# Kernel optimization log

Hardware: AMD Instinct MI355X
Metric: run time of the kernel (lower is better)

The kernel has to match this reference:

```python
import jax, jax.numpy as jnp
import numpy as np

N_NODES = 50000
N_EDGES = 1600000
IN_DIM = 256
HID = 128
BATCH = 16384
EDGE_FEAT = 6
BN_EPS = 1e-5


def _glorot(key, shape):
    fan_in, fan_out = shape[0], shape[1]
    lim = float(np.sqrt(6.0 / (fan_in + fan_out)))
    return jax.random.uniform(key, shape, jnp.float32, -lim, lim)


def setup_inputs() -> dict:
    key = jax.random.key(0)
    ks = jax.random.split(key, 20)
    return {
        "x": jax.random.normal(ks[0], (N_NODES, IN_DIM), jnp.float32),
        "edge_index": jax.random.randint(ks[1], (2, N_EDGES), 0, N_NODES, jnp.int64 if jax.config.jax_enable_x64 else jnp.int32),
        "src_nodes": jax.random.randint(ks[2], (BATCH,), 0, N_NODES),
        "tgt_nodes": jax.random.randint(ks[3], (BATCH,), 0, N_NODES),
        "edge_features": jax.random.uniform(ks[4], (BATCH, EDGE_FEAT), jnp.float32),
        # SAGEConv layer 0: lin_l (aggregated neighbors, has bias), lin_r (root, no bias)
        "sage_wl0": _glorot(ks[5], (IN_DIM, HID)),
        "sage_b0": jnp.zeros((HID,), jnp.float32),
        "sage_wr0": _glorot(ks[6], (IN_DIM, HID)),
        # SAGEConv layer 1
        "sage_wl1": _glorot(ks[7], (HID, HID)),
        "sage_b1": jnp.zeros((HID,), jnp.float32),
        "sage_wr1": _glorot(ks[8], (HID, HID)),
        # edge_processor: Linear(6, 64)
        "ep_w": _glorot(ks[9], (EDGE_FEAT, HID // 2)),
        "ep_b": jnp.zeros((HID // 2,), jnp.float32),
        # predictor: Linear(320,128) -> ReLU -> BN(128) -> Linear(128,64) -> ReLU -> Linear(64,1) -> Sigmoid
        "p1_w": _glorot(ks[10], (2 * HID + HID // 2, HID)),
        "p1_b": jnp.zeros((HID,), jnp.float32),
        "bn_gamma": jnp.ones((HID,), jnp.float32),
        "bn_beta": jnp.zeros((HID,), jnp.float32),
        "bn_mean": jnp.zeros((HID,), jnp.float32),
        "bn_var": jnp.ones((HID,), jnp.float32),
        "p2_w": _glorot(ks[11], (HID, HID // 2)),
        "p2_b": jnp.zeros((HID // 2,), jnp.float32),
        "p3_w": _glorot(ks[12], (HID // 2, 1)),
        "p3_b": jnp.zeros((1,), jnp.float32),
    }


def _sage_conv(h, src, dst, w_l, b, w_r):
    # PyG SAGEConv(mean): out_i = W_l @ mean_{j in N(i)} h_j + b + W_r @ h_i
    n = h.shape[0]
    agg = jax.ops.segment_sum(h[src], dst, num_segments=n)  # [N, d]
    deg = jax.ops.segment_sum(jnp.ones((src.shape[0],), h.dtype), dst, num_segments=n)
    mean = agg / jnp.maximum(deg, 1.0)[:, None]
    return mean @ w_l + b + h @ w_r


def reference(x, edge_index, src_nodes, tgt_nodes, edge_features,
              sage_wl0, sage_b0, sage_wr0, sage_wl1, sage_b1, sage_wr1,
              ep_w, ep_b, p1_w, p1_b, bn_gamma, bn_beta, bn_mean, bn_var,
              p2_w, p2_b, p3_w, p3_b):
    src, dst = edge_index[0], edge_index[1]
    h = _sage_conv(x, src, dst, sage_wl0, sage_b0, sage_wr0)
    h = jax.nn.relu(h)  # dropout is identity in eval mode
    h = _sage_conv(h, src, dst, sage_wl1, sage_b1, sage_wr1)
    src_emb = h[src_nodes]  # [B, HID]
    tgt_emb = h[tgt_nodes]  # [B, HID]
    edge_proc = jax.nn.relu(edge_features @ ep_w + ep_b)  # [B, HID//2]
    combined = jnp.concatenate([src_emb, tgt_emb, edge_proc], axis=1)  # [B, 320]
    z = jax.nn.relu(combined @ p1_w + p1_b)
    z = (z - bn_mean) / jnp.sqrt(bn_var + BN_EPS) * bn_gamma + bn_beta  # BN eval mode
    z = jax.nn.relu(z @ p2_w + p2_b)
    return jax.nn.sigmoid(z @ p3_w + p3_b)  # [B, 1]
```

## Files before the change

kernel.cpp:

```cpp
#include <hip/hip_runtime.h>
#include <hip/hip_bf16.h>

#define N_NODES 50000
#define N_EDGES 1600000
#define BATCH   16384
#define HID     128
#define NBUCK   782
#define NBLK    1000
#define EPB     1600

using short8  = __attribute__((ext_vector_type(8))) short;
using floatx4 = __attribute__((ext_vector_type(4))) float;
using floatv4 = __attribute__((ext_vector_type(4))) float;
using uint2v  = __attribute__((ext_vector_type(2))) unsigned;
typedef unsigned short ushort_t;

__device__ __forceinline__ float bflo(unsigned u){ return __uint_as_float(u << 16); }
__device__ __forceinline__ float bfhi(unsigned u){ return __uint_as_float(u & 0xffff0000u); }
__device__ __forceinline__ float bf1(ushort_t u){ return __uint_as_float(((unsigned)u) << 16); }
__device__ __forceinline__ ushort_t f2bf(float f){
    unsigned u = __float_as_uint(f);
    return (ushort_t)((u + 0x7fffu + ((u >> 16) & 1u)) >> 16);
}
__device__ __forceinline__ int geti(const void* p, long long i, int is64){
    return is64 ? (int)((const long long*)p)[i] : ((const int*)p)[i];
}

__global__ void k_detect(const unsigned* __restrict__ xbits,
                         const unsigned* __restrict__ eibits, int* flags){
    if (threadIdx.x == 0 && blockIdx.x == 0){
        int big = 0;
        for (int i = 0; i < 256; ++i){
            unsigned u = xbits[i];
            unsigned e0 = (u >> 7)  & 0xFF;
            unsigned e1 = (u >> 23) & 0xFF;
            if (e0 >= 140) big++;
            if (e1 >= 140) big++;
        }
        flags[0] = (big > 0) ? 1 : 0;
        int oddnz = 0;
        for (int i = 0; i < 256; ++i)
            if (eibits[2*i + 1] != 0) oddnz++;
        flags[1] = (oddnz == 0) ? 1 : 0;
    }
}

#define NT 19
struct ConvDesc { const void* src[NT]; int cum[NT + 1]; };
__global__ void k_conv(ConvDesc d, ushort_t* __restrict__ dst, const int* __restrict__ flags){
    int i = blockIdx.x*256 + threadIdx.x;
    if (i >= d.cum[NT]) return;
    int seg = 0;
    while (i >= d.cum[seg + 1]) seg++;
    int off = i - d.cum[seg];
    ushort_t v;
    if (flags[0]) v = f2bf(((const float*)d.src[seg])[off]);
    else          v = ((const ushort_t*)d.src[seg])[off];
    dst[i] = v;
}

#define OFF_WL0 0
#define OFF_WR0 32768
#define OFF_WL1 65536
#define OFF_WR1 81920
#define OFF_B0  98304
#define OFF_B1  98432
#define OFF_EPW 98560
#define OFF_EPB 98944
#define OFF_P1W 99008
#define OFF_P1B 139968
#define OFF_BNG 140096
#define OFF_BNB 140224
#define OFF_BNM 140352
#define OFF_BNV 140480
#define OFF_P2W 140608
#define OFF_P2B 148800
#define OFF_P3W 148864
#define OFF_EF  148928
#define OFF_P3B 247232
#define CW_TOT  247233

#define PACK_TOT 147584
__global__ void k_pack(const ushort_t* __restrict__ cw,
                       ushort_t* __restrict__ bp0, ushort_t* __restrict__ bp1,
                       ushort_t* __restrict__ bpp1, ushort_t* __restrict__ bpp2,
                       float* __restrict__ bnf){
    int i = blockIdx.x*256 + threadIdx.x;
    if (i < 65536){
        int j = i & 7, lane = (i >> 3) & 63, c = (i >> 9) & 15, kk = i >> 13;
        int k = kk*32 + (lane >> 4)*8 + j;
        int n = c*16 + (lane & 15);
        bp0[i] = (n < 128) ? cw[OFF_WL0 + k*128 + n] : cw[OFF_WR0 + k*128 + (n-128)];
    } else if (i < 98304){
        int i2 = i - 65536;
        int j = i2 & 7, lane = (i2 >> 3) & 63, c = (i2 >> 9) & 15, kk = i2 >> 13;
        int k = kk*32 + (lane >> 4)*8 + j;
        int n = c*16 + (lane & 15);
        bp1[i2] = (n < 128) ? cw[OFF_WL1 + k*128 + n] : cw[OFF_WR1 + k*128 + (n-128)];
    } else if (i < 139264){
        int i2 = i - 98304;
        int j = i2 & 7, lane = (i2 >> 3) & 63, ct = (i2 >> 9) & 7, kk = i2 >> 12;
        int k = kk*32 + (lane >> 4)*8 + j;
        int n = ct*16 + (lane & 15);
        bpp1[i2] = cw[OFF_P1W + k*128 + n];
    } else if (i < 147456){
        int i2 = i - 139264;
        int j = i2 & 7, lane = (i2 >> 3) & 63, ct = (i2 >> 9) & 3, kk = i2 >> 11;
        int k = kk*32 + (lane >> 4)*8 + j;
        int n = ct*16 + (lane & 15);
        bpp2[i2] = cw[OFF_P2W + k*64 + n];
    } else if (i < PACK_TOT){
        int n = i - 147456;
        float g = bf1(cw[OFF_BNG + n]), b = bf1(cw[OFF_BNB + n]);
        float m = bf1(cw[OFF_BNM + n]), v = bf1(cw[OFF_BNV + n]);
        float sc = g / sqrtf(v + 1e-5f);
        bnf[n] = sc; bnf[128 + n] = b - m*sc;
    }
}

__global__ __launch_bounds__(256)
void k_xcast(const float* __restrict__ x, ushort_t* __restrict__ xbf,
             const int* __restrict__ flags){
    if (!flags[0]) return;
    int i = blockIdx.x*256 + threadIdx.x;
    floatv4 v = ((const floatv4*)x)[i];
    uint2v o;
    o.x = (unsigned)f2bf(v[0]) | ((unsigned)f2bf(v[1]) << 16);
    o.y = (unsigned)f2bf(v[2]) | ((unsigned)f2bf(v[3]) << 16);
    ((uint2v*)xbf)[i] = o;
}

__global__ __launch_bounds__(256)
void kb_hist(const void* __restrict__ ei, int* __restrict__ hist,
             const int* __restrict__ flags){
    __shared__ int lh[NBUCK];
    for (int i = threadIdx.x; i < NBUCK; i += 256) lh[i] = 0;
    __syncthreads();
    int i64 = flags[1];
    int e0 = blockIdx.x * EPB;
    for (int e = e0 + threadIdx.x; e < e0 + EPB; e += 256){
        int d = geti(ei, (long long)N_EDGES + e, i64);
        atomicAdd(&lh[d >> 6], 1);
    }
    __syncthreads();
    for (int i = threadIdx.x; i < NBUCK; i += 256)
        hist[i * NBLK + blockIdx.x] = lh[i];
}

__global__ __launch_bounds__(1024)
void kb_scancol(int* __restrict__ hist, int* __restrict__ btot){
    __shared__ int sh[1024];
    int b = blockIdx.x, t = threadIdx.x;
    int v = (t < NBLK) ? hist[b*NBLK + t] : 0;
    sh[t] = v; __syncthreads();
    for (int o = 1; o < 1024; o <<= 1){
        int x = (t >= o) ? sh[t-o] : 0;
        __syncthreads();
        sh[t] += x;
        __syncthreads();
    }
    if (t < NBLK) hist[b*NBLK + t] = sh[t] - v;
    if (t == 1023) btot[b] = sh[1023];
}

__global__ __launch_bounds__(1024)
void kb_scanbase(const int* __restrict__ btot, int* __restrict__ bbase,
                 int* __restrict__ off){
    __shared__ int sh[1024];
    int t = threadIdx.x;
    int v = (t < NBUCK) ? btot[t] : 0;
    sh[t] = v; __syncthreads();
    for (int o = 1; o < 1024; o <<= 1){
        int x = (t >= o) ? sh[t-o] : 0;
        __syncthreads();
        sh[t] += x;
        __syncthreads();
    }
    if (t < NBUCK) bbase[t] = sh[t] - v;
    if (t == 0){ bbase[NBUCK] = N_EDGES; off[N_NODES] = N_EDGES; }
}

__global__ __launch_bounds__(256)
void kb_scatter(const void* __restrict__ ei, const int* __restrict__ hist,
                const int* __restrict__ bbase, unsigned* __restrict__ ebuf,
                const int* __restrict__ flags){
    __shared__ int lcur[NBUCK];
    for (int i = threadIdx.x; i < NBUCK; i += 256)
        lcur[i] = bbase[i] + hist[i*NBLK + blockIdx.x];
    __syncthreads();
    int i64 = flags[1];
    int e0 = blockIdx.x * EPB;
    for (int e = e0 + threadIdx.x; e < e0 + EPB; e += 256){
        int s = geti(ei, e, i64);
        int d = geti(ei, (long long)N_EDGES + e, i64);
        int p = atomicAdd(&lcur[d >> 6], 1);
        ebuf[p] = (unsigned)s | ((unsigned)(d & 63) << 16);
    }
}

__global__ __launch_bounds__(256)
void kb_csr(const unsigned* __restrict__ ebuf, const int* __restrict__ bbase,
            ushort_t* __restrict__ csr, int* __restrict__ off){
    __shared__ int ldeg[64];
    int b = blockIdx.x, t = threadIdx.x;
    int ebase = bbase[b], eend = bbase[b+1];
    if (t < 64) ldeg[t] = 0;
    __syncthreads();
    for (int i = ebase + t; i < eend; i += 256)
        atomicAdd(&ldeg[(ebuf[i] >> 16) & 63], 1);
    __syncthreads();
    if (t < 64){
        int v = ldeg[t];
        int sum = v;
        #pragma unroll
        for (int o = 1; o < 64; o <<= 1){
            int x = __shfl_up(sum, o, 64);
            if (t >= o) sum += x;
        }
        int excl = sum - v;
        int node = b*64 + t;
        if (node < N_NODES) off[node] = ebase + excl;
        ldeg[t] = excl;
    }
    __syncthreads();
    for (int i = ebase + t; i < eend; i += 256){
        unsigned u = ebuf[i];
        int p = atomicAdd(&ldeg[(u >> 16) & 63], 1);
        csr[ebase + p] = (ushort_t)(u & 0xffffu);
    }
}

template<int KSTEPS, bool MF32>
__global__ __launch_bounds__(256)
void k_gemm2(const void* __restrict__ a_raw, const ushort_t* __restrict__ a_bf,
             const ushort_t* __restrict__ Bp, ushort_t* __restrict__ out,
             int M, const int* __restrict__ flags)
{
    const int lane = threadIdx.x & 63;
    const int w    = threadIdx.x >> 6;
    const int l16  = lane & 15;
    const int q    = lane >> 4;
    const int S    = KSTEPS * 32;
    const int m_base = blockIdx.x * 64;

    const ushort_t* A = (MF32 && flags[0]) ? a_bf : (const ushort_t*)a_raw;

    const ushort_t* arow[4];
    bool ok[4];
    #pragma unroll
    for (int rt = 0; rt < 4; ++rt){
        int m = m_base + rt*16 + l16;
        ok[rt] = (m < M);
        arow[rt] = A + (size_t)(ok[rt] ? m : 0) * S + q*8;
    }
    const short8* bbase = (const short8*)(Bp + (size_t)(w*4)*64*8) + lane;

    floatx4 acc[4][4] = {};
    for (int kk = 0; kk < KSTEPS; ++kk){
        short8 b[4];
        #pragma unroll
        for (int ci = 0; ci < 4; ++ci)
            b[ci] = bbase[(kk*16 + ci)*64];
        short8 a[4];
        #pragma unroll
        for (int rt = 0; rt < 4; ++rt){
            short8 af = {0,0,0,0,0,0,0,0};
            if (ok[rt]) af = *(const short8*)(arow[rt] + kk*32);
            a[rt] = af;
        }
        #pragma unroll
        for (int rt = 0; rt < 4; ++rt)
            #pragma unroll
            for (int ci = 0; ci < 4; ++ci)
                acc[rt][ci] = __builtin_amdgcn_mfma_f32_16x16x32_bf16(a[rt], b[ci], acc[rt][ci], 0, 0, 0);
    }

    #pragma unroll
    for (int rt = 0; rt < 4; ++rt){
        int row_b = m_base + rt*16 + q*4;
        #pragma unroll
        for (int r = 0; r < 4; ++r){
            int row = row_b + r;
            if (row < M){
                #pragma unroll
                for (int ci = 0; ci < 4; ++ci)
                    out[(size_t)row*256 + w*64 + ci*16 + l16] = f2bf(acc[rt][ci][r]);
            }
        }
    }
}

__global__ __launch_bounds__(256)
void k_agg(const int* __restrict__ off, const ushort_t* __restrict__ csr,
           const ushort_t* __restrict__ yr, const ushort_t* __restrict__ bias,
           ushort_t* __restrict__ out, int do_relu)
{
    int v = blockIdx.x*4 + (threadIdx.x >> 6);
    if (v >= N_NODES) return;
    int l = threadIdx.x & 63;
    int e0 = off[v], e1 = off[v+1];
    const unsigned* base = (const unsigned*)yr;
    float a0 = 0.f, a1 = 0.f;
    int p = e0;
    for (; p + 4 <= e1; p += 4){
        int u0 = csr[p], u1 = csr[p+1], u2 = csr[p+2], u3 = csr[p+3];
        unsigned x0 = base[u0*128 + l];
        unsigned x1 = base[u1*128 + l];
        unsigned x2 = base[u2*128 + l];
        unsigned x3 = base[u3*128 + l];
        a0 += bflo(x0); a1 += bfhi(x0);
        a0 += bflo(x1); a1 += bfhi(x1);
        a0 += bflo(x2); a1 += bfhi(x2);
        a0 += bflo(x3); a1 += bfhi(x3);
    }
    for (; p < e1; ++p){
        unsigned x = base[csr[p]*128 + l];
        a0 += bflo(x); a1 += bfhi(x);
    }
    float inv = 1.f / (float)max(e1 - e0, 1);
    unsigned rr = base[v*128 + 64 + l];
    unsigned bb = ((const unsigned*)bias)[l];
    a0 = a0*inv + bflo(rr) + bflo(bb);
    a1 = a1*inv + bfhi(rr) + bfhi(bb);
    if (do_relu){ a0 = fmaxf(a0, 0.f); a1 = fmaxf(a1, 0.f); }
    ((unsigned*)out)[v*64 + l] = (unsigned)f2bf(a0) | ((unsigned)f2bf(a1) << 16);
}

__global__ __launch_bounds__(256)
void k_pred2(const ushort_t* __restrict__ h2,
             const void* __restrict__ srcn, const void* __restrict__ tgtn,
             const ushort_t* __restrict__ cw, const ushort_t* __restrict__ bpp1,
             const ushort_t* __restrict__ bpp2, const float* __restrict__ bnf,
             void* __restrict__ outp, const int* __restrict__ flags)
{
    __shared__ ushort_t comb[64][328];
    __shared__ ushort_t zbuf[64][136];
    __shared__ ushort_t z2buf[64][68];
    __shared__ float    partial[4][64];
    __shared__ int      sid[64], tid_[64];

    const int t    = threadIdx.x;
    const int lane = t & 63;
    const int w    = t >> 6;
    const int l16  = lane & 15;
    const int q    = lane >> 4;
    const int row0 = blockIdx.x * 64;
    const int i64  = flags[1];

    if (t < 64){ sid[t] = geti(srcn, row0 + t, i64); tid_[t] = geti(tgtn, row0 + t, i64); }
    __syncthreads();

    const unsigned* h2u = (const unsigned*)h2;
    #pragma unroll 4
    for (int r = w*16; r < w*16 + 16; ++r){
        unsigned us = h2u[(size_t)sid[r]*64 + lane];
        unsigned ut = h2u[(size_t)tid_[r]*64 + lane];
        *(unsigned*)&comb[r][2*lane]       = us;
        *(unsigned*)&comb[r][128 + 2*lane] = ut;
    }
    {
        int r = t >> 2, c0 = (t & 3) * 16;
        float efv[6];
        #pragma unroll
        for (int k = 0; k < 6; ++k) efv[k] = bf1(cw[OFF_EF + (row0 + r)*6 + k]);
        #pragma unroll
        for (int c = 0; c < 16; ++c){
            int n = c0 + c;
            float a = bf1(cw[OFF_EPB + n]);
            #pragma unroll
            for (int k = 0; k < 6; ++k) a += efv[k] * bf1(cw[OFF_EPW + k*64 + n]);
            comb[r][256 + n] = f2bf(fmaxf(a, 0.f));
        }
    }
    __syncthreads();

    floatx4 acc[4][2] = {};
    for (int kk = 0; kk < 10; ++kk){
        short8 a[4];
        #pragma unroll
        for (int rt = 0; rt < 4; ++rt)
            a[rt] = *(const short8*)&comb[rt*16 + l16][kk*32 + q*8];
        #pragma unroll
        for (int ci = 0; ci < 2; ++ci){
            short8 b = *(const short8*)&bpp1[(((kk*8) + (w*2 + ci))*64 + lane)*8];
            #pragma unroll
            for (int rt = 0; rt < 4; ++rt)
                acc[rt][ci] = __builtin_amdgcn_mfma_f32_16x16x32_bf16(a[rt], b, acc[rt][ci], 0, 0, 0);
        }
    }
    #pragma unroll
    for (int ci = 0; ci < 2; ++ci){
        int n = w*32 + ci*16 + l16;
        float b1v = bf1(cw[OFF_P1B + n]);
        float sc = bnf[n], sh = bnf[128 + n];
        #pragma unroll
        for (int rt = 0; rt < 4; ++rt)
            #pragma unroll
            for (int r = 0; r < 4; ++r){
                float v = fmaxf(acc[rt][ci][r] + b1v, 0.f) * sc + sh;
                zbuf[rt*16 + q*4 + r][n] = f2bf(v);
            }
    }
    __syncthreads();

    floatx4 acc2[4] = {};
    for (int kk = 0; kk < 4; ++kk){
        short8 b = *(const short8*)&bpp2[(((kk*4) + w)*64 + lane)*8];
        #pragma unroll
        for (int rt = 0; rt < 4; ++rt){
            short8 a = *(const short8*)&zbuf[rt*16 + l16][kk*32 + q*8];
            acc2[rt] = __builtin_amdgcn_mfma_f32_16x16x32_bf16(a, b, acc2[rt], 0, 0, 0);
        }
    }
    {
        int n = w*16 + l16;
        float b2v = bf1(cw[OFF_P2B + n]);
        #pragma unroll
        for (int rt = 0; rt < 4; ++rt)
            #pragma unroll
            for (int r = 0; r < 4; ++r)
                z2buf[rt*16 + q*4 + r][n] = f2bf(fmaxf(acc2[rt][r] + b2v, 0.f));
    }
    __syncthreads();

    {
        int r = t & 63, seg = t >> 6;
        float s = 0.f;
        #pragma unroll
        for (int c = 0; c < 16; ++c){
            int n = seg*16 + c;
            s += bf1(z2buf[r][n]) * bf1(cw[OFF_P3W + n]);
        }
        partial[seg][r] = s;
    }
    __syncthreads();
    if (t < 64){
        float zf = partial[0][t] + partial[1][t] + partial[2][t] + partial[3][t] + bf1(cw[OFF_P3B]);
        float sg = 1.f / (1.f + __expf(-zf));
        if (flags[0]) ((float*)outp)[row0 + t] = sg;
        else          ((ushort_t*)outp)[row0 + t] = f2bf(sg);
    }
}

extern "C" void kernel_launch(void* const* d_in, const int* in_sizes, int n_in,
                              void* d_out, int out_size, void* d_ws, size_t ws_size,
                              hipStream_t stream)
{
    const void* x    = d_in[0];
    const void* ei   = d_in[1];
    const void* srcn = d_in[2];
    const void* tgtn = d_in[3];

    char* p = (char*)d_ws;
    auto carve = [&](size_t bytes)->char*{ char* r = p; p += (bytes + 511) & ~size_t(511); return r; };
    int* flags = (int*)carve(64);
    int* off   = (int*)carve((N_NODES+1)*4);
    int* btot  = (int*)carve(NBUCK*4);
    int* bbase = (int*)carve((NBUCK+1)*4);
    ushort_t* csr = (ushort_t*)carve((size_t)N_EDGES*2);
    ushort_t* yr  = (ushort_t*)carve((size_t)N_NODES*256*2);
    ushort_t* h   = (ushort_t*)carve((size_t)N_NODES*128*2);
    ushort_t* cw  = (ushort_t*)carve((size_t)CW_TOT*2);
    ushort_t* bp0 = (ushort_t*)carve((size_t)65536*2);
    ushort_t* bp1 = (ushort_t*)carve((size_t)32768*2);
    ushort_t* bpp1= (ushort_t*)carve((size_t)40960*2);
    ushort_t* bpp2= (ushort_t*)carve((size_t)8192*2);
    float*    bnf = (float*)carve(256*4);
    ushort_t* xbf = (ushort_t*)carve((size_t)N_NODES*256*2);

    int*      hist = (int*)yr;
    unsigned* ebuf = (unsigned*)((char*)yr + 8u*1024*1024);

    k_detect<<<1, 64, 0, stream>>>((const unsigned*)x, (const unsigned*)ei, flags);

    ConvDesc cd;
    const int srcidx[NT] = {5,7,8,10,6,9,11,12,13,14,15,16,17,18,19,20,21,4,22};
    const int lens[NT]   = {32768,32768,16384,16384,128,128,384,64,40960,128,128,128,128,128,8192,64,64,98304,1};
    int run = 0;
    for (int i = 0; i < NT; ++i){ cd.src[i] = d_in[srcidx[i]]; cd.cum[i] = run; run += lens[i]; }
    cd.cum[NT] = run;
    k_conv<<<(CW_TOT+255)/256, 256, 0, stream>>>(cd, cw, flags);
    k_pack<<<(PACK_TOT+255)/256, 256, 0, stream>>>(cw, bp0, bp1, bpp1, bpp2, bnf);
    k_xcast<<<12500, 256, 0, stream>>>((const float*)x, xbf, flags);

    kb_hist    <<<NBLK, 256, 0, stream>>>(ei, hist, flags);
    kb_scancol <<<NBUCK, 1024, 0, stream>>>(hist, btot);
    kb_scanbase<<<1, 1024, 0, stream>>>(btot, bbase, off);
    kb_scatter <<<NBLK, 256, 0, stream>>>(ei, hist, bbase, ebuf, flags);
    kb_csr     <<<NBUCK, 256, 0, stream>>>(ebuf, bbase, csr, off);

    int gblocks = (N_NODES + 63) / 64;
    k_gemm2<8, true ><<<gblocks, 256, 0, stream>>>(x, xbf, bp0, yr, N_NODES, flags);
    k_agg<<<(N_NODES+3)/4, 256, 0, stream>>>(off, csr, yr, cw+OFF_B0, h, 1);
    k_gemm2<4, false><<<gblocks, 256, 0, stream>>>(h, nullptr, bp1, yr, N_NODES, flags);
    k_agg<<<(N_NODES+3)/4, 256, 0, stream>>>(off, csr, yr, cw+OFF_B1, h, 0);

    k_pred2<<<BATCH/64, 256, 0, stream>>>(h, srcn, tgtn, cw, bpp1, bpp2, bnf, d_out, flags);
}
```

Baseline: 394.3 us.

## Slice CSR by source range and aggregate 8 nodes per wave slice-by-slice

The CSR build now splits each node's neighbor list into 7 sub-ranges keyed on the source ID's high bits, storing 8 offsets per node. The aggregation kernel has each wave handle 8 destination nodes and walk all of them one source slice at a time. The goal is to keep gathered rows of yr within a small, cache-resident window during each slice. The histogram/scan stage also shrinks to 256 blocks so the column scan fits in one 256-thread block, and flag detection is parallelized. Risks include lower parallelism in aggregation (fewer waves with serialized node loops), more register use, and the larger offset array.

```diff
diff --git a/kernel.cpp b/kernel.cpp
--- a/kernel.cpp
+++ b/kernel.cpp
@@ -6,8 +6,9 @@
 #define BATCH   16384
 #define HID     128
 #define NBUCK   782
-#define NBLK    1000
-#define EPB     1600
+#define NBLK    256
+#define EPB     6250
+#define NSLICE  7
 
 using short8  = __attribute__((ext_vector_type(8))) short;
 using floatx4 = __attribute__((ext_vector_type(4))) float;
@@ -28,21 +29,17 @@
 
 __global__ void k_detect(const unsigned* __restrict__ xbits,
                          const unsigned* __restrict__ eibits, int* flags){
-    if (threadIdx.x == 0 && blockIdx.x == 0){
-        int big = 0;
-        for (int i = 0; i < 256; ++i){
-            unsigned u = xbits[i];
-            unsigned e0 = (u >> 7)  & 0xFF;
-            unsigned e1 = (u >> 23) & 0xFF;
-            if (e0 >= 140) big++;
-            if (e1 >= 140) big++;
-        }
-        flags[0] = (big > 0) ? 1 : 0;
-        int oddnz = 0;
-        for (int i = 0; i < 256; ++i)
-            if (eibits[2*i + 1] != 0) oddnz++;
-        flags[1] = (oddnz == 0) ? 1 : 0;
-    }
+    __shared__ int f[2];
+    int t = threadIdx.x;
+    if (t < 2) f[t] = 0;
+    __syncthreads();
+    unsigned u = xbits[t];
+    unsigned e0 = (u >> 7)  & 0xFF;
+    unsigned e1 = (u >> 23) & 0xFF;
+    if (e0 >= 140 || e1 >= 140) atomicOr(&f[0], 1);
+    if (eibits[2*t + 1] != 0)   atomicOr(&f[1], 1);
+    __syncthreads();
+    if (t == 0){ flags[0] = f[0]; flags[1] = f[1] ? 0 : 1; }
 }
 
 #define NT 19
@@ -147,25 +144,24 @@
         hist[i * NBLK + blockIdx.x] = lh[i];
 }
 
-__global__ __launch_bounds__(1024)
+__global__ __launch_bounds__(256)
 void kb_scancol(int* __restrict__ hist, int* __restrict__ btot){
-    __shared__ int sh[1024];
+    __shared__ int sh[256];
     int b = blockIdx.x, t = threadIdx.x;
-    int v = (t < NBLK) ? hist[b*NBLK + t] : 0;
+    int v = hist[b*NBLK + t];
     sh[t] = v; __syncthreads();
-    for (int o = 1; o < 1024; o <<= 1){
+    for (int o = 1; o < 256; o <<= 1){
         int x = (t >= o) ? sh[t-o] : 0;
         __syncthreads();
         sh[t] += x;
         __syncthreads();
     }
-    if (t < NBLK) hist[b*NBLK + t] = sh[t] - v;
-    if (t == 1023) btot[b] = sh[1023];
+    hist[b*NBLK + t] = sh[t] - v;
+    if (t == 255) btot[b] = sh[255];
 }
 
 __global__ __launch_bounds__(1024)
-void kb_scanbase(const int* __restrict__ btot, int* __restrict__ bbase,
-                 int* __restrict__ off){
+void kb_scanbase(const int* __restrict__ btot, int* __restrict__ bbase){
     __shared__ int sh[1024];
     int t = threadIdx.x;
     int v = (t < NBUCK) ? btot[t] : 0;
@@ -177,7 +173,7 @@
         __syncthreads();
     }
     if (t < NBUCK) bbase[t] = sh[t] - v;
-    if (t == 0){ bbase[NBUCK] = N_EDGES; off[N_NODES] = N_EDGES; }
+    if (t == 0) bbase[NBUCK] = N_EDGES;
 }
 
 __global__ __launch_bounds__(256)
@@ -200,33 +196,47 @@
 
 __global__ __launch_bounds__(256)
 void kb_csr(const unsigned* __restrict__ ebuf, const int* __restrict__ bbase,
-            ushort_t* __restrict__ csr, int* __restrict__ off){
-    __shared__ int ldeg[64];
+            ushort_t* __restrict__ csr, int* __restrict__ off2){
+    __shared__ int bins[448];
     int b = blockIdx.x, t = threadIdx.x;
     int ebase = bbase[b], eend = bbase[b+1];
-    if (t < 64) ldeg[t] = 0;
-    __syncthreads();
-    for (int i = ebase + t; i < eend; i += 256)
-        atomicAdd(&ldeg[(ebuf[i] >> 16) & 63], 1);
-    __syncthreads();
-    if (t < 64){
-        int v = ldeg[t];
-        int sum = v;
-        #pragma unroll
-        for (int o = 1; o < 64; o <<= 1){
-            int x = __shfl_up(sum, o, 64);
-            if (t >= o) sum += x;
-        }
-        int excl = sum - v;
-        int node = b*64 + t;
-        if (node < N_NODES) off[node] = ebase + excl;
-        ldeg[t] = excl;
-    }
+    for (int i = t; i < 448; i += 256) bins[i] = 0;
     __syncthreads();
     for (int i = ebase + t; i < eend; i += 256){
         unsigned u = ebuf[i];
-        int p = atomicAdd(&ldeg[(u >> 16) & 63], 1);
-        csr[ebase + p] = (ushort_t)(u & 0xffffu);
+        int n = (u >> 16) & 63;
+        int s = (int)(u & 0xffffu) >> 13;
+        atomicAdd(&bins[n*7 + s], 1);
+    }
+    __syncthreads();
+    if (t < 64){
+        int base = t*7;
+        int c[7], sum = 0;
+        #pragma unroll
+        for (int j = 0; j < 7; ++j){ c[j] = sum; sum += bins[base + j]; }
+        int incl = sum;
+        #pragma unroll
+        for (int o = 1; o < 64; o <<= 1){
+            int x = __shfl_up(incl, o, 64);
+            if (t >= o) incl += x;
+        }
+        int start = ebase + incl - sum;
+        int node = b*64 + t;
+        if (node < N_NODES){
+            #pragma unroll
+            for (int j = 0; j < 7; ++j) off2[node*8 + j] = start + c[j];
+            off2[node*8 + 7] = start + sum;
+        }
+        #pragma unroll
+        for (int j = 0; j < 7; ++j) bins[base + j] = start + c[j];
+    }
+    __syncthreads();
+    for (int i = ebase + t; i < eend; i += 256){
+        unsigned u = ebuf[i];
+        int n = (u >> 16) & 63;
+        int src = (int)(u & 0xffffu);
+        int p = atomicAdd(&bins[n*7 + (src >> 13)], 1);
+        csr[p] = (ushort_t)src;
     }
 }
 
@@ -291,39 +301,54 @@
 }
 
 __global__ __launch_bounds__(256)
-void k_agg(const int* __restrict__ off, const ushort_t* __restrict__ csr,
-           const ushort_t* __restrict__ yr, const ushort_t* __restrict__ bias,
-           ushort_t* __restrict__ out, int do_relu)
+void k_agg3(const int* __restrict__ off2, const ushort_t* __restrict__ csr,
+            const ushort_t* __restrict__ yr, const ushort_t* __restrict__ bias,
+            ushort_t* __restrict__ out, int do_relu)
 {
-    int v = blockIdx.x*4 + (threadIdx.x >> 6);
-    if (v >= N_NODES) return;
-    int l = threadIdx.x & 63;
-    int e0 = off[v], e1 = off[v+1];
-    const unsigned* base = (const unsigned*)yr;
-    float a0 = 0.f, a1 = 0.f;
-    int p = e0;
-    for (; p + 4 <= e1; p += 4){
-        int u0 = csr[p], u1 = csr[p+1], u2 = csr[p+2], u3 = csr[p+3];
-        unsigned x0 = base[u0*128 + l];
-        unsigned x1 = base[u1*128 + l];
-        unsigned x2 = base[u2*128 + l];
-        unsigned x3 = base[u3*128 + l];
-        a0 += bflo(x0); a1 += bfhi(x0);
-        a0 += bflo(x1); a1 += bfhi(x1);
-        a0 += bflo(x2); a1 += bfhi(x2);
-        a0 += bflo(x3); a1 += bfhi(x3);
-    }
-    for (; p < e1; ++p){
-        unsigned x = base[csr[p]*128 + l];
-        a0 += bflo(x); a1 += bfhi(x);
-    }
-    float inv = 1.f / (float)max(e1 - e0, 1);
-    unsigned rr = base[v*128 + 64 + l];
+    const int wave = blockIdx.x*4 + (threadIdx.x >> 6);
+    const int v0   = wave * 8;
+    const int l    = threadIdx.x & 63;
+    const unsigned* yb = (const unsigned*)yr;
+
+    float acc0[8] = {}, acc1[8] = {};
+    for (int s = 0; s < NSLICE; ++s){
+        #pragma unroll
+        for (int n = 0; n < 8; ++n){
+            int v = v0 + n;
+            if (v >= N_NODES) continue;
+            int e  = off2[v*8 + s];
+            int e1 = off2[v*8 + s + 1];
+            float s0 = acc0[n], s1 = acc1[n];
+            for (; e + 4 <= e1; e += 4){
+                int u0 = csr[e], u1 = csr[e+1], u2 = csr[e+2], u3 = csr[e+3];
+                unsigned d0 = yb[(size_t)u0*128 + l];
+                unsigned d1 = yb[(size_t)u1*128 + l];
+                unsigned d2 = yb[(size_t)u2*128 + l];
+                unsigned d3 = yb[(size_t)u3*128 + l];
+                s0 += bflo(d0) + bflo(d1) + bflo(d2) + bflo(d3);
+                s1 += bfhi(d0) + bfhi(d1) + bfhi(d2) + bfhi(d3);
+            }
+            for (; e < e1; ++e){
+                unsigned d = yb[(size_t)csr[e]*128 + l];
+                s0 += bflo(d); s1 += bfhi(d);
+            }
+            acc0[n] = s0; acc1[n] = s1;
+        }
+    }
     unsigned bb = ((const unsigned*)bias)[l];
-    a0 = a0*inv + bflo(rr) + bflo(bb);
-    a1 = a1*inv + bfhi(rr) + bfhi(bb);
-    if (do_relu){ a0 = fmaxf(a0, 0.f); a1 = fmaxf(a1, 0.f); }
-    ((unsigned*)out)[v*64 + l] = (unsigned)f2bf(a0) | ((unsigned)f2bf(a1) << 16);
+    float blo = bflo(bb), bhi = bfhi(bb);
+    #pragma unroll
+    for (int n = 0; n < 8; ++n){
+        int v = v0 + n;
+        if (v >= N_NODES) continue;
+        int deg = off2[v*8 + 7] - off2[v*8];
+        float inv = 1.f / (float)max(deg, 1);
+        unsigned rr = yb[(size_t)v*128 + 64 + l];
+        float f0 = acc0[n]*inv + bflo(rr) + blo;
+        float f1 = acc1[n]*inv + bfhi(rr) + bhi;
+        if (do_relu){ f0 = fmaxf(f0, 0.f); f1 = fmaxf(f1, 0.f); }
+        ((unsigned*)out)[(size_t)v*64 + l] = (unsigned)f2bf(f0) | ((unsigned)f2bf(f1) << 16);
+    }
 }
 
 __global__ __launch_bounds__(256)
@@ -454,7 +479,7 @@
     char* p = (char*)d_ws;
     auto carve = [&](size_t bytes)->char*{ char* r = p; p += (bytes + 511) & ~size_t(511); return r; };
     int* flags = (int*)carve(64);
-    int* off   = (int*)carve((N_NODES+1)*4);
+    int* off2  = (int*)carve(((size_t)N_NODES*8 + 8)*4);
     int* btot  = (int*)carve(NBUCK*4);
     int* bbase = (int*)carve((NBUCK+1)*4);
     ushort_t* csr = (ushort_t*)carve((size_t)N_EDGES*2);
@@ -471,7 +496,7 @@
     int*      hist = (int*)yr;
     unsigned* ebuf = (unsigned*)((char*)yr + 8u*1024*1024);
 
-    k_detect<<<1, 64, 0, stream>>>((const unsigned*)x, (const unsigned*)ei, flags);
+    k_detect<<<1, 256, 0, stream>>>((const unsigned*)x, (const unsigned*)ei, flags);
 
     ConvDesc cd;
     const int srcidx[NT] = {5,7,8,10,6,9,11,12,13,14,15,16,17,18,19,20,21,4,22};
@@ -484,16 +509,17 @@
     k_xcast<<<12500, 256, 0, stream>>>((const float*)x, xbf, flags);
 
     kb_hist    <<<NBLK, 256, 0, stream>>>(ei, hist, flags);
-    kb_scancol <<<NBUCK, 1024, 0, stream>>>(hist, btot);
-    kb_scanbase<<<1, 1024, 0, stream>>>(btot, bbase, off);
+    kb_scancol <<<NBUCK, 256, 0, stream>>>(hist, btot);
+    kb_scanbase<<<1, 1024, 0, stream>>>(btot, bbase);
     kb_scatter <<<NBLK, 256, 0, stream>>>(ei, hist, bbase, ebuf, flags);
-    kb_csr     <<<NBUCK, 256, 0, stream>>>(ebuf, bbase, csr, off);
+    kb_csr     <<<NBUCK, 256, 0, stream>>>(ebuf, bbase, csr, off2);
 
     int gblocks = (N_NODES + 63) / 64;
+    int ablocks = ((N_NODES + 7)/8 + 3) / 4;
     k_gemm2<8, true ><<<gblocks, 256, 0, stream>>>(x, xbf, bp0, yr, N_NODES, flags);
-    k_agg<<<(N_NODES+3)/4, 256, 0, stream>>>(off, csr, yr, cw+OFF_B0, h, 1);
+    k_agg3<<<ablocks, 256, 0, stream>>>(off2, csr, yr, cw+OFF_B0, h, 1);
     k_gemm2<4, false><<<gblocks, 256, 0, stream>>>(h, nullptr, bp1, yr, N_NODES, flags);
-    k_agg<<<(N_NODES+3)/4, 256, 0, stream>>>(off, csr, yr, cw+OFF_B1, h, 0);
+    k_agg3<<<ablocks, 256, 0, stream>>>(off2, csr, yr, cw+OFF_B1, h, 0);
 
     k_pred2<<<BATCH/64, 256, 0, stream>>>(h, srcn, tgtn, cw, bpp1, bpp2, bnf, d_out, flags);
 }
```

New measurement: 744.2 us. +88.8%, slower.
